# Optimization experiments

Measured on AMD Instinct MI355X. Metric: run time of the kernel, lower is better.

Reference implementation:

```python
import jax, jax.numpy as jnp
import numpy as np

S, K, O = 8192, 1024, 4096  # seq_len, in_features, out_features


def setup_inputs() -> dict:
    key = jax.random.key(0)
    k1, k2, k3, k4, k5 = jax.random.split(key, 5)
    x = jax.random.randint(k1, (S, K), -128, 128, dtype=jnp.int8)
    weight_q = jax.random.randint(k2, (O, K), -128, 128, dtype=jnp.int8)
    scale_x = jax.random.uniform(k3, (), jnp.float32, 0.01, 0.1)
    scale_w = jax.random.uniform(k4, (), jnp.float32, 0.01, 0.1)
    scale_y = jax.random.uniform(k5, (S,), jnp.float32, 0.5, 2.0)  # per-row output scale
    return {"x": x, "weight_q": weight_q, "scale_x": scale_x,
            "scale_w": scale_w, "scale_y": scale_y}


def reference(x, weight_q, scale_x, scale_w, scale_y):
    # int8 GEMM with int32 accumulation: [S,K] @ [O,K]^T -> [S,O]
    acc = jnp.einsum('sk,ok->so', x.astype(jnp.int32), weight_q.astype(jnp.int32))
    # fused per-row requantization: scale_y[:seq_len] gives per-row scale
    requant_scale = (scale_x * scale_w / scale_y).astype(jnp.float32)  # [S]
    scaled = acc.astype(jnp.float32) * requant_scale[:, None]
    out_q = jnp.clip(jnp.round(scaled), -128.0, 127.0).astype(jnp.int8)
    return out_q, scale_y
```

## Files before the change

kernel.cpp:

```cpp
#include <hip/hip_runtime.h>


#define S_DIM 8192
#define K_DIM 1024
#define O_DIM 4096
#define BM 128
#define BN 128
#define BK 64
#define NITER (K_DIM / BK)

using i32x4 = __attribute__((ext_vector_type(4))) int;

__device__ __forceinline__ void load_lds16(const void* g, void* l) {
  __builtin_amdgcn_global_load_lds(
      (const __attribute__((address_space(1))) void*)g,
      (__attribute__((address_space(3))) void*)l, 16, 0, 0);
}

__global__ void pack_kernel(const int* __restrict__ xi, const int* __restrict__ wi,
                            const float* __restrict__ sy,
                            unsigned int* __restrict__ xq, unsigned int* __restrict__ wq,
                            float* __restrict__ out_sy) {
  const int idx = blockIdx.x * blockDim.x + threadIdx.x;
  const int nx = S_DIM * K_DIM / 4;
  const int nw = O_DIM * K_DIM / 4;
  if (idx < nx) {
    int4 v = ((const int4*)xi)[idx];
    unsigned int p = (v.x & 0xff) | ((v.y & 0xff) << 8) |
                     ((v.z & 0xff) << 16) | ((unsigned)(v.w & 0xff) << 24);
    xq[idx] = p;
  } else if (idx < nx + nw) {
    const int j = idx - nx;
    int4 v = ((const int4*)wi)[j];
    unsigned int p = (v.x & 0xff) | ((v.y & 0xff) << 8) |
                     ((v.z & 0xff) << 16) | ((unsigned)(v.w & 0xff) << 24);
    wq[j] = p;
  }
  if (idx < S_DIM) out_sy[idx] = sy[idx];
}

__global__ __launch_bounds__(256, 4) void gemm_i8_kernel(
    const signed char* __restrict__ A,
    const signed char* __restrict__ B,
    const float* __restrict__ sx, const float* __restrict__ sw,
    const float* __restrict__ sy, float* __restrict__ out) {
  __shared__ __align__(16) signed char As[2][BM * BK];
  __shared__ __align__(16) signed char Bs[2][BN * BK];

  const int tid = threadIdx.x;
  const int wave = tid >> 6;
  const int lane = tid & 63;
  const int wm = wave >> 1;
  const int wn = wave & 1;
  const int rowBase = blockIdx.x * BM;
  const int colBase = blockIdx.y * BN;

  const int sRow = wave * 16 + (lane >> 2);
  const int sCol = (((lane & 3) ^ ((lane >> 2) & 3))) * 16;
  const signed char* gA = A + (size_t)(rowBase + sRow) * K_DIM + sCol;
  const signed char* gB = B + (size_t)(colBase + sRow) * K_DIM + sCol;

  i32x4 acc[4][4] = {};

  const int fr = lane & 15;
  const int fq = (((lane >> 4) ^ (fr & 3)) & 3) * 16;

  {
    signed char* lA = As[0] + wave * 1024;
    signed char* lB = Bs[0] + wave * 1024;
    load_lds16(gA, lA);
    load_lds16(gA + (size_t)64 * K_DIM, lA + 4096);
    load_lds16(gB, lB);
    load_lds16(gB + (size_t)64 * K_DIM, lB + 4096);
  }

  for (int it = 0; it < NITER; ++it) {
    __syncthreads();

    if (it + 1 < NITER) {
      const int nb = (it + 1) & 1;
      const int k0 = (it + 1) * BK;
      signed char* lA = As[nb] + wave * 1024;
      signed char* lB = Bs[nb] + wave * 1024;
      load_lds16(gA + k0, lA);
      load_lds16(gA + (size_t)64 * K_DIM + k0, lA + 4096);
      load_lds16(gB + k0, lB);
      load_lds16(gB + (size_t)64 * K_DIM + k0, lB + 4096);
    }

    const signed char* curA = As[it & 1];
    const signed char* curB = Bs[it & 1];
    i32x4 bf[4];
#pragma unroll
    for (int ni = 0; ni < 4; ++ni)
      bf[ni] = *(const i32x4*)(curB + (wn * 64 + ni * 16 + fr) * BK + fq);

#pragma unroll
    for (int mi = 0; mi < 4; ++mi) {
      i32x4 af = *(const i32x4*)(curA + (wm * 64 + mi * 16 + fr) * BK + fq);
#pragma unroll
      for (int ni = 0; ni < 4; ++ni)
        acc[mi][ni] =
            __builtin_amdgcn_mfma_i32_16x16x64_i8(af, bf[ni], acc[mi][ni], 0, 0, 0);
    }
  }

  const float sxw = sx[0] * sw[0];
  const int quad = lane >> 4;
#pragma unroll
  for (int mi = 0; mi < 4; ++mi) {
#pragma unroll
    for (int r = 0; r < 4; ++r) {
      const int s = rowBase + wm * 64 + mi * 16 + quad * 4 + r;
      const float rs = sxw / sy[s];
      float* orow = out + (size_t)s * O_DIM + colBase + wn * 64 + fr;
#pragma unroll
      for (int ni = 0; ni < 4; ++ni) {
        float f = rintf((float)acc[mi][ni][r] * rs);
        f = fminf(127.0f, fmaxf(-128.0f, f));
        orow[ni * 16] = f;
      }
    }
  }
}

extern "C" void kernel_launch(void* const* d_in, const int* in_sizes, int n_in,
                              void* d_out, int out_size, void* d_ws, size_t ws_size,
                              hipStream_t stream) {
  const int* x = (const int*)d_in[0];
  const int* w = (const int*)d_in[1];
  const float* sx = (const float*)d_in[2];
  const float* sw = (const float*)d_in[3];
  const float* sy = (const float*)d_in[4];
  float* out = (float*)d_out;

  unsigned int* xq = (unsigned int*)d_ws;
  unsigned int* wq = xq + (size_t)S_DIM * K_DIM / 4;

  const int total = S_DIM * K_DIM / 4 + O_DIM * K_DIM / 4;
  pack_kernel<<<(total + 255) / 256, 256, 0, stream>>>(
      x, w, sy, xq, wq, out + (size_t)S_DIM * O_DIM);

  dim3 grid(S_DIM / BM, O_DIM / BN);
  gemm_i8_kernel<<<grid, 256, 0, stream>>>(
      (const signed char*)xq, (const signed char*)wq, sx, sw, sy, out);
}
```

Baseline: 205.3 us.

## Pre-pack int8 operands into tile-contiguous swizzled layout for contiguous LDS loads

The pack kernel now writes A and B as 128x64 tiles stored contiguously, with the LDS swizzle already applied. Each thread handles 16 packed bytes instead of 4. The GEMM then streams each K-step tile as one contiguous 8KB block per operand, so global-to-LDS loads are fully coalesced instead of strided across 1KB rows. The cost is more index arithmetic and a scattered read pattern in the pack kernel, plus a layout hard-coded to the tile shape.

```diff
diff --git a/kernel.cpp b/kernel.cpp
--- a/kernel.cpp
+++ b/kernel.cpp
@@ -8,6 +8,7 @@
 #define BN 128
 #define BK 64
 #define NITER (K_DIM / BK)
+#define TILE_BYTES (BM * BK)
 
 using i32x4 = __attribute__((ext_vector_type(4))) int;
 
@@ -19,33 +20,48 @@
 
 __global__ void pack_kernel(const int* __restrict__ xi, const int* __restrict__ wi,
                             const float* __restrict__ sy,
-                            unsigned int* __restrict__ xq, unsigned int* __restrict__ wq,
+                            uint4* __restrict__ ap, uint4* __restrict__ bp,
                             float* __restrict__ out_sy) {
-  const int idx = blockIdx.x * blockDim.x + threadIdx.x;
-  const int nx = S_DIM * K_DIM / 4;
-  const int nw = O_DIM * K_DIM / 4;
-  if (idx < nx) {
-    int4 v = ((const int4*)xi)[idx];
-    unsigned int p = (v.x & 0xff) | ((v.y & 0xff) << 8) |
-                     ((v.z & 0xff) << 16) | ((unsigned)(v.w & 0xff) << 24);
-    xq[idx] = p;
-  } else if (idx < nx + nw) {
-    const int j = idx - nx;
-    int4 v = ((const int4*)wi)[j];
-    unsigned int p = (v.x & 0xff) | ((v.y & 0xff) << 8) |
-                     ((v.z & 0xff) << 16) | ((unsigned)(v.w & 0xff) << 24);
-    wq[j] = p;
+  const int tid = blockIdx.x * blockDim.x + threadIdx.x;
+  const int nA = S_DIM * K_DIM / 16;
+  const int nB = O_DIM * K_DIM / 16;
+
+  const int* src;
+  uint4* dst;
+  int j;
+  if (tid < nA) {
+    src = xi; dst = ap; j = tid;
+  } else if (tid < nA + nB) {
+    src = wi; dst = bp; j = tid - nA;
+  } else {
+    return;
   }
-  if (idx < S_DIM) out_sy[idx] = sy[idx];
+  const int t = j >> 9;
+  const int idx = j & 511;
+  const int r = idx >> 2;
+  const int cs = idx & 3;
+  const int c = cs ^ (r & 3);
+  const int band = t >> 4;
+  const int kt = t & 15;
+  const int row = band * 128 + r;
+  const int4* s4 = (const int4*)src + row * 256 + kt * 16 + c * 4;
+  int4 v0 = s4[0], v1 = s4[1], v2 = s4[2], v3 = s4[3];
+  uint4 o;
+  o.x = (v0.x & 0xff) | ((v0.y & 0xff) << 8) | ((v0.z & 0xff) << 16) | (((unsigned)v0.w & 0xff) << 24);
+  o.y = (v1.x & 0xff) | ((v1.y & 0xff) << 8) | ((v1.z & 0xff) << 16) | (((unsigned)v1.w & 0xff) << 24);
+  o.z = (v2.x & 0xff) | ((v2.y & 0xff) << 8) | ((v2.z & 0xff) << 16) | (((unsigned)v2.w & 0xff) << 24);
+  o.w = (v3.x & 0xff) | ((v3.y & 0xff) << 8) | ((v3.z & 0xff) << 16) | (((unsigned)v3.w & 0xff) << 24);
+  dst[j] = o;
+  if (tid < S_DIM) out_sy[tid] = sy[tid];
 }
 
 __global__ __launch_bounds__(256, 4) void gemm_i8_kernel(
-    const signed char* __restrict__ A,
-    const signed char* __restrict__ B,
+    const signed char* __restrict__ Ap,
+    const signed char* __restrict__ Bp,
     const float* __restrict__ sx, const float* __restrict__ sw,
     const float* __restrict__ sy, float* __restrict__ out) {
-  __shared__ __align__(16) signed char As[2][BM * BK];
-  __shared__ __align__(16) signed char Bs[2][BN * BK];
+  __shared__ __align__(16) signed char As[2][TILE_BYTES];
+  __shared__ __align__(16) signed char Bs[2][TILE_BYTES];
 
   const int tid = threadIdx.x;
   const int wave = tid >> 6;
@@ -55,37 +71,32 @@
   const int rowBase = blockIdx.x * BM;
   const int colBase = blockIdx.y * BN;
 
-  const int sRow = wave * 16 + (lane >> 2);
-  const int sCol = (((lane & 3) ^ ((lane >> 2) & 3))) * 16;
-  const signed char* gA = A + (size_t)(rowBase + sRow) * K_DIM + sCol;
-  const signed char* gB = B + (size_t)(colBase + sRow) * K_DIM + sCol;
+  const int soff = wave * 1024 + lane * 16;
+  const signed char* gA = Ap + (size_t)blockIdx.x * NITER * TILE_BYTES + soff;
+  const signed char* gB = Bp + (size_t)blockIdx.y * NITER * TILE_BYTES + soff;
+  signed char* ldsA = (signed char*)As + wave * 1024;
+  signed char* ldsB = (signed char*)Bs + wave * 1024;
 
   i32x4 acc[4][4] = {};
 
   const int fr = lane & 15;
   const int fq = (((lane >> 4) ^ (fr & 3)) & 3) * 16;
 
-  {
-    signed char* lA = As[0] + wave * 1024;
-    signed char* lB = Bs[0] + wave * 1024;
-    load_lds16(gA, lA);
-    load_lds16(gA + (size_t)64 * K_DIM, lA + 4096);
-    load_lds16(gB, lB);
-    load_lds16(gB + (size_t)64 * K_DIM, lB + 4096);
-  }
+  load_lds16(gA, ldsA);
+  load_lds16(gA + 4096, ldsA + 4096);
+  load_lds16(gB, ldsB);
+  load_lds16(gB + 4096, ldsB + 4096);
 
   for (int it = 0; it < NITER; ++it) {
     __syncthreads();
 
     if (it + 1 < NITER) {
-      const int nb = (it + 1) & 1;
-      const int k0 = (it + 1) * BK;
-      signed char* lA = As[nb] + wave * 1024;
-      signed char* lB = Bs[nb] + wave * 1024;
-      load_lds16(gA + k0, lA);
-      load_lds16(gA + (size_t)64 * K_DIM + k0, lA + 4096);
-      load_lds16(gB + k0, lB);
-      load_lds16(gB + (size_t)64 * K_DIM + k0, lB + 4096);
+      const int boff = ((it + 1) & 1) * TILE_BYTES;
+      const size_t goff = (size_t)(it + 1) * TILE_BYTES;
+      load_lds16(gA + goff, ldsA + boff);
+      load_lds16(gA + goff + 4096, ldsA + boff + 4096);
+      load_lds16(gB + goff, ldsB + boff);
+      load_lds16(gB + goff + 4096, ldsB + boff + 4096);
     }
 
     const signed char* curA = As[it & 1];
@@ -134,14 +145,14 @@
   const float* sy = (const float*)d_in[4];
   float* out = (float*)d_out;
 
-  unsigned int* xq = (unsigned int*)d_ws;
-  unsigned int* wq = xq + (size_t)S_DIM * K_DIM / 4;
+  uint4* ap = (uint4*)d_ws;
+  uint4* bp = ap + (size_t)S_DIM * K_DIM / 16;
 
-  const int total = S_DIM * K_DIM / 4 + O_DIM * K_DIM / 4;
+  const int total = S_DIM * K_DIM / 16 + O_DIM * K_DIM / 16;
   pack_kernel<<<(total + 255) / 256, 256, 0, stream>>>(
-      x, w, sy, xq, wq, out + (size_t)S_DIM * O_DIM);
+      x, w, sy, ap, bp, out + (size_t)S_DIM * O_DIM);
 
   dim3 grid(S_DIM / BM, O_DIM / BN);
   gemm_i8_kernel<<<grid, 256, 0, stream>>>(
-      (const signed char*)xq, (const signed char*)wq, sx, sw, sy, out);
+      (const signed char*)ap, (const signed char*)bp, sx, sw, sy, out);
 }
```

Result: faster. 200.9 us (-2.1%).
